# Optimization experiments

Measured on AMD Instinct MI355X. Metric: run time of the kernel, lower is better.

## Reference

```python
import jax, jax.numpy as jnp
import numpy as np

B, S, H = 8, 2048, 1024
CHUNK = 64
INTER = 2048
BASE_LR = 0.01
MAX_GRAD_NORM = 1.0
EPS = 1e-6


def rmsnorm(x, w):
    return x * jax.lax.rsqrt(jnp.mean(x * x, axis=-1, keepdims=True) + EPS) * w


def mem_fwd(params, x):
    # 2-layer MLP memory with residual: x + RMSNorm(W1 @ silu(W0 @ x))
    w0, w1, ln = params
    h = jax.nn.silu(x @ w0.T)
    y = h @ w1.T
    return x + rmsnorm(y, ln)


def forward(x, wq_w, wk_w, wv_w, q_norm_w, k_norm_w, alpha_w, theta_w, eta_w, mem_w0, mem_w1, mem_ln_w):
    Bx, Sx, Hx = x.shape
    NC = Sx // CHUNK  # seq_len divisible by chunk_size here (no padding needed)
    xc = x.reshape(Bx, NC, CHUNK, Hx)
    xf = xc.reshape(Bx, NC, CHUNK * Hx)

    # adaptive coefficients per chunk
    alpha = jax.nn.sigmoid(jnp.mean(xf @ alpha_w.T, axis=0))   # (NC, 1)
    theta = jax.nn.sigmoid(xf @ theta_w.T) * BASE_LR           # (B, NC, 1) per-sample loss weights
    eta = jax.nn.sigmoid(jnp.mean(xf @ eta_w.T, axis=0))       # (NC, 1)
    beta = 1.0 - alpha

    k = rmsnorm(jax.nn.silu(xc @ wk_w.T), k_norm_w)  # (B, NC, C, H)
    v = jax.nn.silu(xc @ wv_w.T)                     # (B, NC, C, H)

    mem0 = (mem_w0, mem_w1, mem_ln_w)
    surp0 = jax.tree_util.tree_map(jnp.zeros_like, mem0)

    def step(carry, inp):
        mem, surp = carry
        k_c, v_c, th_c, eta_c, beta_c = inp  # k_c,v_c: (B,C,H); th_c: (B,1); eta_c,beta_c: (1,)

        def loss_fn(p):
            pred = mem_fwd(p, k_c)
            return jnp.mean((v_c - pred) ** 2 * th_c[:, :, None])

        grads = jax.grad(loss_fn)(mem)
        total = jnp.sqrt(sum(jnp.sum(g * g) for g in grads))
        clip = jax.lax.stop_gradient(jnp.minimum(MAX_GRAD_NORM / (total + 1e-6), 1.0))
        new_surp = tuple(eta_c * s_ - g * clip for s_, g in zip(surp, grads))
        new_mem = tuple(beta_c * m + ns for m, ns in zip(mem, new_surp))
        return (new_mem, new_surp), None

    xs = (jnp.swapaxes(k, 0, 1), jnp.swapaxes(v, 0, 1), jnp.swapaxes(theta, 0, 1), eta, beta)
    (mem_f, _), _ = jax.lax.scan(step, (mem0, surp0), xs)

    # retrieve with final memory weights
    q = rmsnorm(jax.nn.silu(x @ wq_w.T), q_norm_w)
    return mem_fwd(mem_f, q)


def setup_inputs() -> dict:
    key = jax.random.key(0)
    ks = jax.random.split(key, 9)
    s = 0.02
    return {
        "x": jax.random.normal(ks[0], (B, S, H), jnp.float32),
        "wq_w": jax.random.normal(ks[1], (H, H), jnp.float32) * s,
        "wk_w": jax.random.normal(ks[2], (H, H), jnp.float32) * s,
        "wv_w": jax.random.normal(ks[3], (H, H), jnp.float32) * s,
        "q_norm_w": jnp.ones((H,), jnp.float32),
        "k_norm_w": jnp.ones((H,), jnp.float32),
        "alpha_w": jax.random.normal(ks[4], (1, CHUNK * H), jnp.float32) * s,
        "theta_w": jax.random.normal(ks[5], (1, CHUNK * H), jnp.float32) * s,
        "eta_w": jax.random.normal(ks[6], (1, CHUNK * H), jnp.float32) * s,
        "mem_w0": jax.random.normal(ks[7], (INTER, H), jnp.float32) * s,
        "mem_w1": jax.random.normal(ks[8], (H, INTER), jnp.float32) * s,
        "mem_ln_w": jnp.ones((H,), jnp.float32),
    }


def reference(x, wq_w, wk_w, wv_w, q_norm_w, k_norm_w, alpha_w, theta_w, eta_w, mem_w0, mem_w1, mem_ln_w):
    return forward(x, wq_w, wk_w, wv_w, q_norm_w, k_norm_w, alpha_w, theta_w, eta_w, mem_w0, mem_w1, mem_ln_w)
```

## Files before the change

### kernel.cpp

```cpp
#include <hip/hip_runtime.h>

#define HD 1024
#define ID 2048
#define NCHUNK 32
#define CHUNKSZ 64
#define NB 8
#define SEQ 2048
#define ROWS 512
#define MTOT 524288.0f
#define EPSF 1e-6f

typedef unsigned short u16;
typedef unsigned int u32;
typedef short bf16x8 __attribute__((ext_vector_type(8)));
typedef float f32x4 __attribute__((ext_vector_type(4)));

#define GATHER(r, c) ((((r) >> 6) * SEQ) + ((c) * CHUNKSZ) + ((r) & 63))

__device__ __forceinline__ float sigmoidf_(float x) { return 1.f / (1.f + expf(-x)); }
__device__ __forceinline__ float siluf_(float x)    { return x / (1.f + expf(-x)); }
__device__ __forceinline__ float silu_d_(float z)   { float sg = sigmoidf_(z); return sg * (1.f + z * (1.f - sg)); }

__device__ __forceinline__ u16 f2b(float f) {
  union { float f; u32 u; } v; v.f = f;
  return (u16)((v.u + 0x7fffu + ((v.u >> 16) & 1u)) >> 16);
}
__device__ __forceinline__ float b2f(u16 b) {
  union { u32 u; float f; } v; v.u = ((u32)b) << 16; return v.f;
}
__device__ __forceinline__ u32 pack2(float a, float b) { return (u32)f2b(a) | ((u32)f2b(b) << 16); }

__device__ __forceinline__ float block_reduce_sum(float v, float* s4) {
  #pragma unroll
  for (int off = 32; off > 0; off >>= 1) v += __shfl_down(v, off);
  int lane = threadIdx.x & 63, wid = threadIdx.x >> 6;
  if (lane == 0) s4[wid] = v;
  __syncthreads();
  float r = s4[0] + s4[1] + s4[2] + s4[3];
  __syncthreads();
  return r;
}

template<bool T>
__device__ __forceinline__ void stage64(u16* S, int srow, int c16, const uint4& r0, const uint4& r1) {
  if (!T) {
    *(uint4*)(S + srow * 72 + c16)     = r0;
    *(uint4*)(S + srow * 72 + c16 + 8) = r1;
  } else {
    const u16* e0 = (const u16*)&r0;
    const u16* e1 = (const u16*)&r1;
    #pragma unroll
    for (int e = 0; e < 8; ++e) S[(c16 + e) * 72 + srow] = e0[e];
    #pragma unroll
    for (int e = 0; e < 8; ++e) S[(c16 + 8 + e) * 72 + srow] = e1[e];
  }
}

template<bool AT, bool BT>
__device__ __forceinline__ void gemm64_db(
    f32x4 (&acc)[2][2], const u16* __restrict__ A, const u16* __restrict__ B,
    int K, int m0, int n0, int lda, int ldb, int chA, int chB,
    u16* As, u16* Bs)
{
  const int tid = threadIdx.x;
  const int lane = tid & 63, wave = tid >> 6;
  const int wr = wave >> 1, wc = wave & 1;
  const int l15 = lane & 15, q = lane >> 4;
  const int srow = tid >> 2, c16 = (tid & 3) * 16;

  const u16* Ap; size_t Astep;
  if (!AT) {
    int r = m0 + srow;
    if (chA >= 0) r = GATHER(r, chA);
    Ap = A + (size_t)r * lda + c16;
    Astep = 64;
  } else {
    Ap = A + (size_t)srow * lda + m0 + c16;
    Astep = (size_t)64 * lda;
  }
  const u16* Bp; size_t Bstep;
  if (!BT) {
    Bp = B + (size_t)(n0 + srow) * ldb + c16;
    Bstep = 64;
  } else {
    if (chB >= 0) { Bp = B + ((size_t)chB * CHUNKSZ + srow) * ldb + n0 + c16; Bstep = (size_t)SEQ * ldb; }
    else          { Bp = B + (size_t)srow * ldb + n0 + c16;                   Bstep = (size_t)64 * ldb; }
  }

  uint4 ra0 = *(const uint4*)Ap, ra1 = *(const uint4*)(Ap + 8);
  uint4 rb0 = *(const uint4*)Bp, rb1 = *(const uint4*)(Bp + 8);
  stage64<AT>(As, srow, c16, ra0, ra1);
  stage64<BT>(Bs, srow, c16, rb0, rb1);

  const int nt = K >> 6;
  int cur = 0;
  for (int t = 0; t < nt; ++t) {
    if (t + 1 < nt) {
      Ap += Astep; Bp += Bstep;
      ra0 = *(const uint4*)Ap; ra1 = *(const uint4*)(Ap + 8);
      rb0 = *(const uint4*)Bp; rb1 = *(const uint4*)(Bp + 8);
    }
    __syncthreads();
    const u16* Ac = As + cur * (64 * 72);
    const u16* Bc = Bs + cur * (64 * 72);
    #pragma unroll
    for (int ks = 0; ks < 2; ++ks) {
      bf16x8 af[2], bg[2];
      #pragma unroll
      for (int i = 0; i < 2; ++i) af[i] = *(const bf16x8*)&Ac[(wr * 32 + i * 16 + l15) * 72 + ks * 32 + q * 8];
      #pragma unroll
      for (int j = 0; j < 2; ++j) bg[j] = *(const bf16x8*)&Bc[(wc * 32 + j * 16 + l15) * 72 + ks * 32 + q * 8];
      #pragma unroll
      for (int i = 0; i < 2; ++i)
        #pragma unroll
        for (int j = 0; j < 2; ++j)
          acc[i][j] = __builtin_amdgcn_mfma_f32_16x16x32_bf16(af[i], bg[j], acc[i][j], 0, 0, 0);
    }
    if (t + 1 < nt) {
      stage64<AT>(As + (cur ^ 1) * (64 * 72), srow, c16, ra0, ra1);
      stage64<BT>(Bs + (cur ^ 1) * (64 * 72), srow, c16, rb0, rb1);
    }
    cur ^= 1;
  }
}

__global__ __launch_bounds__(256) void gemm64_fwd(
    float* __restrict__ C, u16* __restrict__ Cb,
    const u16* __restrict__ A, const u16* __restrict__ B, int N, int K, int chunk)
{
  __shared__ __align__(16) u16 As[2 * 64 * 72];
  __shared__ __align__(16) u16 Bs[2 * 64 * 72];
  const int m0 = blockIdx.y * 64, n0 = blockIdx.x * 64;
  f32x4 acc[2][2] = {};
  gemm64_db<false, false>(acc, A, B, K, m0, n0, K, K, chunk, -1, As, Bs);
  const int lane = threadIdx.x & 63, wave = threadIdx.x >> 6;
  const int wr = wave >> 1, wc = wave & 1;
  const int l15 = lane & 15, q = lane >> 4;
  #pragma unroll
  for (int i = 0; i < 2; ++i) {
    int r = m0 + wr * 32 + i * 16 + q * 4;
    #pragma unroll
    for (int j = 0; j < 2; ++j) {
      int col = n0 + wc * 32 + j * 16 + l15;
      #pragma unroll
      for (int t = 0; t < 4; ++t) {
        float v = acc[i][j][t];
        size_t o = (size_t)(r + t) * N + col;
        C[o] = v;
        Cb[o] = f2b(siluf_(v));
      }
    }
  }
}

__global__ __launch_bounds__(256) void gemm64_dh(
    u16* __restrict__ Cb, const u16* __restrict__ A, const u16* __restrict__ B,
    const float* __restrict__ Z, int N, int K)
{
  __shared__ __align__(16) u16 As[2 * 64 * 72];
  __shared__ __align__(16) u16 Bs[2 * 64 * 72];
  const int m0 = blockIdx.y * 64, n0 = blockIdx.x * 64;
  f32x4 acc[2][2] = {};
  gemm64_db<false, true>(acc, A, B, K, m0, n0, K, N, -1, -1, As, Bs);
  const int lane = threadIdx.x & 63, wave = threadIdx.x >> 6;
  const int wr = wave >> 1, wc = wave & 1;
  const int l15 = lane & 15, q = lane >> 4;
  #pragma unroll
  for (int i = 0; i < 2; ++i) {
    int r = m0 + wr * 32 + i * 16 + q * 4;
    #pragma unroll
    for (int j = 0; j < 2; ++j) {
      int col = n0 + wc * 32 + j * 16 + l15;
      #pragma unroll
      for (int t = 0; t < 4; ++t) {
        size_t o = (size_t)(r + t) * N + col;
        Cb[o] = f2b(acc[i][j][t] * silu_d_(Z[o]));
      }
    }
  }
}

__global__ __launch_bounds__(256) void gemm_grads(
    float* __restrict__ Gw1, const u16* __restrict__ dY, const u16* __restrict__ hfw,
    float* __restrict__ Gw0, const u16* __restrict__ dH, const u16* __restrict__ kall,
    int c, const float* __restrict__ g, const float* __restrict__ y,
    const float* __restrict__ srow, float* __restrict__ Gln, float* __restrict__ nsqc)
{
  __shared__ __align__(16) u16 As[2 * 64 * 72];
  __shared__ __align__(16) u16 Bs[2 * 64 * 72];
  __shared__ float s4[4];
  int bid = blockIdx.x;
  const int tid = threadIdx.x;
  if (bid >= 1024) {
    int j = (bid - 1024) * 32 + (tid & 31);
    int rg = tid >> 5;
    float acc = 0.f;
    #pragma unroll 4
    for (int i = 0; i < 64; ++i) {
      int r = rg * 64 + i;
      size_t o = (size_t)r * HD + j;
      acc += g[o] * y[o] * srow[r];
    }
    float* part = (float*)As;
    part[rg * 32 + (tid & 31)] = acc;
    __syncthreads();
    if (tid < 32) {
      float tot = 0.f;
      #pragma unroll
      for (int k = 0; k < 8; ++k) tot += part[k * 32 + tid];
      Gln[j] = tot;
      float sq = tot * tot;
      #pragma unroll
      for (int off = 16; off > 0; off >>= 1) sq += __shfl_down(sq, off);
      if (tid == 0) atomicAdd(nsqc, sq);
    }
    return;
  }
  float* C; const u16* A; const u16* B; int N, m0, n0, lda, ldb, chB;
  if (bid < 512) { A = dY; B = hfw;  C = Gw1; N = ID; lda = HD; ldb = ID; chB = -1; m0 = (bid >> 5) * 64; n0 = (bid & 31) * 64; }
  else { bid -= 512; A = dH; B = kall; C = Gw0; N = HD; lda = ID; ldb = HD; chB = c; m0 = (bid >> 4) * 64; n0 = (bid & 15) * 64; }
  f32x4 acc[2][2] = {};
  gemm64_db<true, true>(acc, A, B, ROWS, m0, n0, lda, ldb, -1, chB, As, Bs);
  const int lane = tid & 63, wave = tid >> 6;
  const int wr = wave >> 1, wc = wave & 1;
  const int l15 = lane & 15, q = lane >> 4;
  float ssq = 0.f;
  #pragma unroll
  for (int i = 0; i < 2; ++i) {
    int r = m0 + wr * 32 + i * 16 + q * 4;
    #pragma unroll
    for (int j = 0; j < 2; ++j) {
      int col = n0 + wc * 32 + j * 16 + l15;
      #pragma unroll
      for (int t = 0; t < 4; ++t) {
        float v = acc[i][j][t];
        C[(size_t)(r + t) * N + col] = v;
        ssq += v * v;
      }
    }
  }
  float tot = block_reduce_sum(ssq, s4);
  if (tid == 0) atomicAdd(nsqc, tot);
}

__global__ __launch_bounds__(128) void gemm_y32(
    float* __restrict__ C, const u16* __restrict__ A, const u16* __restrict__ B,
    int N, int K)
{
  __shared__ __align__(16) u16 As[2 * 32 * 72];
  __shared__ __align__(16) u16 Bs[2 * 64 * 72];
  const int tid = threadIdx.x;
  const int lane = tid & 63, wc = tid >> 6;
  const int l15 = lane & 15, q = lane >> 4;
  const int m0 = blockIdx.y * 32, n0 = blockIdx.x * 64;

  const int arow = tid >> 2, ac16 = (tid & 3) * 16;
  const int brow = tid >> 1, bc32 = (tid & 1) * 32;
  const u16* Ap = A + (size_t)(m0 + arow) * K + ac16;
  const u16* Bp = B + (size_t)(n0 + brow) * K + bc32;

  uint4 ra0 = *(const uint4*)Ap, ra1 = *(const uint4*)(Ap + 8);
  uint4 rb0 = *(const uint4*)Bp, rb1 = *(const uint4*)(Bp + 8);
  uint4 rb2 = *(const uint4*)(Bp + 16), rb3 = *(const uint4*)(Bp + 24);
  {
    u16* Aw = As + arow * 72 + ac16;
    u16* Bw = Bs + brow * 72 + bc32;
    *(uint4*)Aw = ra0; *(uint4*)(Aw + 8) = ra1;
    *(uint4*)Bw = rb0; *(uint4*)(Bw + 8) = rb1;
    *(uint4*)(Bw + 16) = rb2; *(uint4*)(Bw + 24) = rb3;
  }

  f32x4 acc[2][2] = {};
  const int nt = K >> 6;
  int cur = 0;
  for (int t = 0; t < nt; ++t) {
    if (t + 1 < nt) {
      Ap += 64; Bp += 64;
      ra0 = *(const uint4*)Ap; ra1 = *(const uint4*)(Ap + 8);
      rb0 = *(const uint4*)Bp; rb1 = *(const uint4*)(Bp + 8);
      rb2 = *(const uint4*)(Bp + 16); rb3 = *(const uint4*)(Bp + 24);
    }
    __syncthreads();
    const u16* Ac = As + cur * (32 * 72);
    const u16* Bc = Bs + cur * (64 * 72);
    #pragma unroll
    for (int ks = 0; ks < 2; ++ks) {
      bf16x8 af[2], bg[2];
      #pragma unroll
      for (int i = 0; i < 2; ++i) af[i] = *(const bf16x8*)&Ac[(i * 16 + l15) * 72 + ks * 32 + q * 8];
      #pragma unroll
      for (int j = 0; j < 2; ++j) bg[j] = *(const bf16x8*)&Bc[(wc * 32 + j * 16 + l15) * 72 + ks * 32 + q * 8];
      #pragma unroll
      for (int i = 0; i < 2; ++i)
        #pragma unroll
        for (int j = 0; j < 2; ++j)
          acc[i][j] = __builtin_amdgcn_mfma_f32_16x16x32_bf16(af[i], bg[j], acc[i][j], 0, 0, 0);
    }
    if (t + 1 < nt) {
      u16* Aw = As + (cur ^ 1) * (32 * 72) + arow * 72 + ac16;
      u16* Bw = Bs + (cur ^ 1) * (64 * 72) + brow * 72 + bc32;
      *(uint4*)Aw = ra0; *(uint4*)(Aw + 8) = ra1;
      *(uint4*)Bw = rb0; *(uint4*)(Bw + 8) = rb1;
      *(uint4*)(Bw + 16) = rb2; *(uint4*)(Bw + 24) = rb3;
    }
    cur ^= 1;
  }
  #pragma unroll
  for (int i = 0; i < 2; ++i) {
    int r = m0 + i * 16 + q * 4;
    #pragma unroll
    for (int j = 0; j < 2; ++j) {
      int col = n0 + wc * 32 + j * 16 + l15;
      #pragma unroll
      for (int t = 0; t < 4; ++t)
        C[(size_t)(r + t) * N + col] = acc[i][j][t];
    }
  }
}

template<int EPI, bool AF32>
__global__ __launch_bounds__(256) void gemm128_t(
    float* __restrict__ C, u16* __restrict__ Cb, u16* __restrict__ Cb1,
    const u16* __restrict__ A, const float* __restrict__ Af,
    const u16* __restrict__ B0, const u16* __restrict__ B1,
    int M, int N, int K)
{
  __shared__ __align__(16) u16 As[128 * 40];
  __shared__ __align__(16) u16 Bs[128 * 40];
  const int tid = threadIdx.x;
  const int lane = tid & 63, wave = tid >> 6;
  const int wr = wave >> 1, wc = wave & 1;
  const int l15 = lane & 15, q = lane >> 4;
  const int m0 = blockIdx.y * 128, n0 = blockIdx.x * 128;
  const u16* B = (EPI == 2 && blockIdx.z) ? B1 : B0;

  f32x4 acc[4][4] = {};
  for (int k0 = 0; k0 < K; k0 += 32) {
    #pragma unroll
    for (int it = 0; it < 2; ++it) {
      int cid = tid + it * 256;
      int row = cid >> 2, c8 = (cid & 3) * 8;
      if (AF32) {
        const float* ap = Af + (size_t)(m0 + row) * K + k0 + c8;
        float4 f0 = *(const float4*)ap;
        float4 f1 = *(const float4*)(ap + 4);
        uint4 o; o.x = pack2(f0.x, f0.y); o.y = pack2(f0.z, f0.w);
        o.z = pack2(f1.x, f1.y); o.w = pack2(f1.z, f1.w);
        *(uint4*)&As[row * 40 + c8] = o;
      } else {
        *(uint4*)&As[row * 40 + c8] = *(const uint4*)&A[(size_t)(m0 + row) * K + k0 + c8];
      }
      *(uint4*)&Bs[row * 40 + c8] = *(const uint4*)&B[(size_t)(n0 + row) * K + k0 + c8];
    }
    __syncthreads();
    bf16x8 af[4], bg[4];
    #pragma unroll
    for (int i = 0; i < 4; ++i) af[i] = *(const bf16x8*)&As[(wr * 64 + i * 16 + l15) * 40 + q * 8];
    #pragma unroll
    for (int j = 0; j < 4; ++j) bg[j] = *(const bf16x8*)&Bs[(wc * 64 + j * 16 + l15) * 40 + q * 8];
    #pragma unroll
    for (int i = 0; i < 4; ++i)
      #pragma unroll
      for (int j = 0; j < 4; ++j)
        acc[i][j] = __builtin_amdgcn_mfma_f32_16x16x32_bf16(af[i], bg[j], acc[i][j], 0, 0, 0);
    __syncthreads();
  }
  #pragma unroll
  for (int i = 0; i < 4; ++i) {
    int r = m0 + wr * 64 + i * 16 + q * 4;
    #pragma unroll
    for (int j = 0; j < 4; ++j) {
      int col = n0 + wc * 64 + j * 16 + l15;
      #pragma unroll
      for (int t = 0; t < 4; ++t) {
        float v = acc[i][j][t];
        size_t o = (size_t)(r + t) * N + col;
        if (EPI == 0) C[o] = v;
        if (EPI == 1) Cb[o] = f2b(siluf_(v));
        if (EPI == 2) { if (blockIdx.z == 0) Cb[o] = f2b(v); else Cb1[o] = f2b(siluf_(v)); }
      }
    }
  }
}

__global__ __launch_bounds__(256) void conv_f2b(u16* __restrict__ dst, const float* __restrict__ src, int n) {
  int i = (blockIdx.x * 256 + threadIdx.x) * 4;
  if (i < n) {
    float4 v = *(const float4*)&src[i];
    uint2 o; o.x = pack2(v.x, v.y); o.y = pack2(v.z, v.w);
    *(uint2*)&dst[i] = o;
  }
}

__global__ __launch_bounds__(256) void dots_kernel(
    const float* __restrict__ x, const float* __restrict__ aw,
    const float* __restrict__ tw, const float* __restrict__ ew,
    float* __restrict__ dA, float* __restrict__ dT, float* __restrict__ dE)
{
  int b = blockIdx.x >> 5, c = blockIdx.x & 31;
  const float* base = x + ((size_t)b * SEQ + (size_t)c * CHUNKSZ) * HD;
  float a = 0.f, t = 0.f, e = 0.f;
  for (int it = 0; it < 64; ++it) {
    int j = (it * 256 + threadIdx.x) * 4;
    float4 xv = *(const float4*)&base[j];
    float4 av = *(const float4*)&aw[j];
    float4 tv = *(const float4*)&tw[j];
    float4 ev = *(const float4*)&ew[j];
    a += xv.x * av.x + xv.y * av.y + xv.z * av.z + xv.w * av.w;
    t += xv.x * tv.x + xv.y * tv.y + xv.z * tv.z + xv.w * tv.w;
    e += xv.x * ev.x + xv.y * ev.y + xv.z * ev.z + xv.w * ev.w;
  }
  __shared__ float s4[4];
  a = block_reduce_sum(a, s4);
  t = block_reduce_sum(t, s4);
  e = block_reduce_sum(e, s4);
  if (threadIdx.x == 0) { dA[blockIdx.x] = a; dT[blockIdx.x] = t; dE[blockIdx.x] = e; }
}

__global__ __launch_bounds__(256) void coeff_kernel(
    const float* __restrict__ dA, const float* __restrict__ dT, const float* __restrict__ dE,
    float* __restrict__ betaA, float* __restrict__ etaA, float* __restrict__ thetaA)
{
  int t = threadIdx.x;
  if (t < 256) thetaA[t] = sigmoidf_(dT[t]) * 0.01f;
  if (t < 32) {
    float sa = 0.f, se = 0.f;
    for (int b = 0; b < NB; ++b) { sa += dA[b * 32 + t]; se += dE[b * 32 + t]; }
    betaA[t] = 1.f - sigmoidf_(sa / 8.f);
    etaA[t]  = sigmoidf_(se / 8.f);
  }
}

template<bool SRCB>
__global__ __launch_bounds__(256) void post_norm(
    u16* __restrict__ dstb, const float* __restrict__ srcf,
    const u16* __restrict__ srcb, const float* __restrict__ nw)
{
  size_t off = (size_t)blockIdx.x * HD;
  float sv[4]; float ss = 0.f;
  #pragma unroll
  for (int i = 0; i < 4; ++i) {
    int j = i * 256 + threadIdx.x;
    float z = SRCB ? b2f(srcb[off + j]) : srcf[off + j];
    float s = siluf_(z);
    sv[i] = s; ss += s * s;
  }
  __shared__ float s4[4];
  ss = block_reduce_sum(ss, s4);
  float rs = rsqrtf(ss / (float)HD + EPSF);
  #pragma unroll
  for (int i = 0; i < 4; ++i) {
    int j = i * 256 + threadIdx.x;
    dstb[off + j] = f2b(sv[i] * rs * nw[j]);
  }
}

__global__ __launch_bounds__(256) void loss_grad(
    const float* __restrict__ y, const u16* __restrict__ kall, const u16* __restrict__ vall,
    const float* __restrict__ ln, const float* __restrict__ thetaA, int c,
    float* __restrict__ g, u16* __restrict__ dYbf, float* __restrict__ srow)
{
  int r = blockIdx.x;
  size_t off = (size_t)r * HD;
  size_t goff = (size_t)GATHER(r, c) * HD;
  float th = thetaA[(r >> 6) * 32 + c];
  float yv[4], lnv[4];
  float ss = 0.f;
  #pragma unroll
  for (int i = 0; i < 4; ++i) {
    int j = i * 256 + threadIdx.x;
    yv[i] = y[off + j];
    lnv[i] = ln[j];
    ss += yv[i] * yv[i];
  }
  __shared__ float s4[4];
  ss = block_reduce_sum(ss, s4);
  float s = rsqrtf(ss / (float)HD + EPSF);
  float coef = 2.f * th / MTOT;
  float gv[4]; float t = 0.f;
  #pragma unroll
  for (int i = 0; i < 4; ++i) {
    int j = i * 256 + threadIdx.x;
    float pred = b2f(kall[goff + j]) + yv[i] * s * lnv[i];
    float gg = coef * (pred - b2f(vall[goff + j]));
    gv[i] = gg;
    g[off + j] = gg;
    t += gg * lnv[i] * yv[i];
  }
  t = block_reduce_sum(t, s4);
  float c3 = s * s * s * t * (1.f / (float)HD);
  #pragma unroll
  for (int i = 0; i < 4; ++i) {
    int j = i * 256 + threadIdx.x;
    dYbf[off + j] = f2b(s * gv[i] * lnv[i] - c3 * yv[i]);
  }
  if (threadIdx.x == 0) srow[r] = s;
}

__global__ __launch_bounds__(256) void update_all(
    float* __restrict__ mw0, float* __restrict__ sw0, const float* __restrict__ g0, u16* __restrict__ w0b,
    float* __restrict__ mw1, float* __restrict__ sw1, const float* __restrict__ g1, u16* __restrict__ w1b,
    float* __restrict__ mln, float* __restrict__ sln, const float* __restrict__ gl,
    const float* __restrict__ etaA, const float* __restrict__ betaA, int c,
    const float* __restrict__ nsqc)
{
  float clip = fminf(1.0f / (sqrtf(*nsqc) + 1e-6f), 1.0f);
  float eta = etaA[c], beta = betaA[c];
  int bid = blockIdx.x;
  if (bid < 2048) {
    float* mw; float* sw; const float* g; u16* wb; size_t i0;
    if (bid < 1024) { mw = mw1; sw = sw1; g = g1; wb = w1b; i0 = (size_t)bid * 2048; }
    else            { mw = mw0; sw = sw0; g = g0; wb = w0b; i0 = (size_t)(bid - 1024) * 2048; }
    i0 += (size_t)threadIdx.x * 8;
    u16 bb[8];
    #pragma unroll
    for (int h = 0; h < 2; ++h) {
      size_t i = i0 + h * 4;
      float4 s = *(float4*)&sw[i];
      float4 gg = *(const float4*)&g[i];
      float4 m = *(float4*)&mw[i];
      s.x = eta * s.x - clip * gg.x; m.x = beta * m.x + s.x;
      s.y = eta * s.y - clip * gg.y; m.y = beta * m.y + s.y;
      s.z = eta * s.z - clip * gg.z; m.z = beta * m.z + s.z;
      s.w = eta * s.w - clip * gg.w; m.w = beta * m.w + s.w;
      *(float4*)&sw[i] = s;
      *(float4*)&mw[i] = m;
      bb[h * 4 + 0] = f2b(m.x); bb[h * 4 + 1] = f2b(m.y);
      bb[h * 4 + 2] = f2b(m.z); bb[h * 4 + 3] = f2b(m.w);
    }
    *(uint4*)&wb[i0] = *(uint4*)bb;
  } else {
    int i = threadIdx.x * 4;
    #pragma unroll
    for (int k = 0; k < 4; ++k) {
      float ns = eta * sln[i + k] - clip * gl[i + k];
      sln[i + k] = ns;
      mln[i + k] = beta * mln[i + k] + ns;
    }
  }
}

__global__ __launch_bounds__(256) void final_out_kernel(
    float* __restrict__ out, const float* __restrict__ zq, const float* __restrict__ y2,
    const float* __restrict__ qn, const float* __restrict__ ln)
{
  size_t off = (size_t)blockIdx.x * HD;
  float sv[4], yv[4];
  float ss1 = 0.f, ss2 = 0.f;
  #pragma unroll
  for (int i = 0; i < 4; ++i) {
    int j = i * 256 + threadIdx.x;
    float s = siluf_(zq[off + j]);
    sv[i] = s; ss1 += s * s;
    yv[i] = y2[off + j];
    ss2 += yv[i] * yv[i];
  }
  __shared__ float s4[4];
  ss1 = block_reduce_sum(ss1, s4);
  ss2 = block_reduce_sum(ss2, s4);
  float rs1 = rsqrtf(ss1 / (float)HD + EPSF);
  float rs2 = rsqrtf(ss2 / (float)HD + EPSF);
  #pragma unroll
  for (int i = 0; i < 4; ++i) {
    int j = i * 256 + threadIdx.x;
    out[off + j] = sv[i] * rs1 * qn[j] + yv[i] * rs2 * ln[j];
  }
}

extern "C" void kernel_launch(void* const* d_in, const int* in_sizes, int n_in,
                              void* d_out, int out_size, void* d_ws, size_t ws_size,
                              hipStream_t stream) {
  const float* x   = (const float*)d_in[0];
  const float* wq  = (const float*)d_in[1];
  const float* wk  = (const float*)d_in[2];
  const float* wv  = (const float*)d_in[3];
  const float* qn  = (const float*)d_in[4];
  const float* kn  = (const float*)d_in[5];
  const float* aw  = (const float*)d_in[6];
  const float* tw  = (const float*)d_in[7];
  const float* ew  = (const float*)d_in[8];
  const float* w0i = (const float*)d_in[9];
  const float* w1i = (const float*)d_in[10];
  const float* lni = (const float*)d_in[11];
  float* out = (float*)d_out;

  float* p = (float*)d_ws;
  auto alloc = [&](size_t n) { n = (n + 63) & ~(size_t)63; float* r = p; p += n; return r; };
  float* memW0  = alloc((size_t)ID * HD);
  float* memW1  = alloc((size_t)HD * ID);
  float* memLn  = alloc(HD);
  float* surpW0 = alloc((size_t)ID * HD);
  float* surpW1 = alloc((size_t)HD * ID);
  float* surpLn = alloc(HD);
  float* Gw0    = alloc((size_t)ID * HD);
  float* Gw1    = alloc((size_t)HD * ID);
  float* Gln    = alloc(HD);
  float* zfw    = alloc((size_t)ROWS * ID);
  float* ybuf   = alloc((size_t)ROWS * HD);
  float* gbuf   = alloc((size_t)ROWS * HD);
  float* srow   = alloc(ROWS);
  float* dotA   = alloc(256);
  float* dotT   = alloc(256);
  float* dotE   = alloc(256);
  float* betaA  = alloc(64);
  float* etaA   = alloc(64);
  float* thetaA = alloc(256);
  float* nsq    = alloc(64);

  u16* bp = (u16*)p;
  auto balloc = [&](size_t n) { n = (n + 63) & ~(size_t)63; u16* r = bp; bp += n; return r; };
  u16* wq_bf  = balloc((size_t)HD * HD);
  u16* wk_bf  = balloc((size_t)HD * HD);
  u16* wv_bf  = balloc((size_t)HD * HD);
  u16* W0_bf  = balloc((size_t)ID * HD);
  u16* W1_bf  = balloc((size_t)HD * ID);
  u16* k_all  = balloc((size_t)NB * SEQ * HD);
  u16* v_all  = balloc((size_t)NB * SEQ * HD);
  u16* hfw_bf = balloc((size_t)ROWS * ID);
  u16* dY_bf  = balloc((size_t)ROWS * HD);
  u16* dH_bf  = balloc((size_t)ROWS * ID);
  size_t needed = (size_t)((char*)bp - (char*)d_ws);
  if (needed > ws_size) return;

  u16* zk_all = (u16*)surpW0;

  conv_f2b<<<(HD * HD) / 1024, 256, 0, stream>>>(wq_bf, wq, HD * HD);
  conv_f2b<<<(HD * HD) / 1024, 256, 0, stream>>>(wk_bf, wk, HD * HD);
  conv_f2b<<<(HD * HD) / 1024, 256, 0, stream>>>(wv_bf, wv, HD * HD);
  conv_f2b<<<(ID * HD) / 1024, 256, 0, stream>>>(W0_bf, w0i, ID * HD);
  conv_f2b<<<(HD * ID) / 1024, 256, 0, stream>>>(W1_bf, w1i, HD * ID);
  dots_kernel<<<256, 256, 0, stream>>>(x, aw, tw, ew, dotA, dotT, dotE);
  coeff_kernel<<<1, 256, 0, stream>>>(dotA, dotT, dotE, betaA, etaA, thetaA);
  gemm128_t<2, true><<<dim3(HD / 128, (NB * SEQ) / 128, 2), 256, 0, stream>>>(
      nullptr, zk_all, v_all, nullptr, x, wk_bf, wv_bf, NB * SEQ, HD, HD);
  post_norm<true><<<NB * SEQ, 256, 0, stream>>>(k_all, nullptr, zk_all, kn);
  hipMemcpyAsync(memW0, w0i, (size_t)ID * HD * 4, hipMemcpyDeviceToDevice, stream);
  hipMemcpyAsync(memW1, w1i, (size_t)HD * ID * 4, hipMemcpyDeviceToDevice, stream);
  hipMemcpyAsync(memLn, lni, (size_t)HD * 4, hipMemcpyDeviceToDevice, stream);
  hipMemsetAsync(surpW0, 0, ((size_t)ID * HD * 2 + HD + 64) * 4, stream);
  hipMemsetAsync(nsq, 0, 64 * 4, stream);

  for (int c = 0; c < NCHUNK; ++c) {
    gemm64_fwd<<<dim3(ID / 64, ROWS / 64), 256, 0, stream>>>(
        zfw, hfw_bf, k_all, W0_bf, ID, HD, c);
    gemm_y32<<<dim3(HD / 64, ROWS / 32), 128, 0, stream>>>(ybuf, hfw_bf, W1_bf, HD, ID);
    loss_grad<<<ROWS, 256, 0, stream>>>(ybuf, k_all, v_all, memLn, thetaA, c, gbuf, dY_bf, srow);
    gemm64_dh<<<dim3(ID / 64, ROWS / 64), 256, 0, stream>>>(
        dH_bf, dY_bf, W1_bf, zfw, ID, HD);
    gemm_grads<<<1056, 256, 0, stream>>>(
        Gw1, dY_bf, hfw_bf, Gw0, dH_bf, k_all, c, gbuf, ybuf, srow, Gln, nsq + c);
    update_all<<<2049, 256, 0, stream>>>(
        memW0, surpW0, Gw0, W0_bf, memW1, surpW1, Gw1, W1_bf,
        memLn, surpLn, Gln, etaA, betaA, c, nsq + c);
  }

  const int RB = 4096;
  float* zq    = surpW0;
  u16*   qb_bf = (u16*)zfw;
  u16*   h_bf  = k_all;
  float* y2    = Gw0;
  for (int blk = 0; blk < (NB * SEQ) / RB; ++blk) {
    const float* xb = x + (size_t)blk * RB * HD;
    gemm128_t<0, true><<<dim3(HD / 128, RB / 128), 256, 0, stream>>>(
        zq, nullptr, nullptr, nullptr, xb, wq_bf, nullptr, RB, HD, HD);
    post_norm<false><<<RB, 256, 0, stream>>>(qb_bf, zq, nullptr, qn);
    gemm128_t<1, false><<<dim3(ID / 128, RB / 128), 256, 0, stream>>>(
        nullptr, h_bf, nullptr, qb_bf, nullptr, W0_bf, nullptr, RB, ID, HD);
    gemm128_t<0, false><<<dim3(HD / 128, RB / 128), 256, 0, stream>>>(
        y2, nullptr, nullptr, h_bf, nullptr, W1_bf, nullptr, RB, HD, ID);
    final_out_kernel<<<RB, 256, 0, stream>>>(out + (size_t)blk * RB * HD, zq, y2, qn, memLn);
  }
}
```

Measured before the change: 3.698 ms.

## Split-K the per-chunk GEMMs and fuse the Q/K/V projections

The per-chunk forward, dh and y GEMMs now use larger blocks that split the K dimension across two or four thread groups and reduce the partial sums through shared memory. This is meant to put more waves to work on the small 512-row scan GEMMs, at the cost of extra LDS traffic and barriers. Separately, x is converted to bf16 once and the Q, K and V projections run in one XCD-aware GEMM launch; the q norm is computed early and stored in the output buffer. The retrieval GEMMs are then processed in larger row blocks using specialised kernels.

```diff
diff --git a/kernel.cpp b/kernel.cpp
--- a/kernel.cpp
+++ b/kernel.cpp
@@ -124,57 +124,152 @@
   }
 }
 
-__global__ __launch_bounds__(256) void gemm64_fwd(
+template<bool BT>
+__device__ __forceinline__ void gemm64x8(
+    f32x4 (&acc)[2][2], const u16* __restrict__ A, const u16* __restrict__ B,
+    int K, int m0, int n0, int lda, int ldb, int chA, u16* As, u16* Bs)
+{
+  const int tid = threadIdx.x;
+  const int half = tid >> 8;
+  const int t2 = tid & 255;
+  const int lane = tid & 63;
+  const int w2 = t2 >> 6;
+  const int wr = w2 >> 1, wc = w2 & 1;
+  const int l15 = lane & 15, q = lane >> 4;
+  const int srow = t2 >> 2, c16 = (t2 & 3) * 16;
+  const int kbase = half * (K >> 1);
+
+  int arow = m0 + srow;
+  if (chA >= 0) arow = GATHER(arow, chA);
+  const u16* Ap = A + (size_t)arow * lda + kbase + c16;
+  const u16* Bp; size_t Bstep;
+  if (!BT) { Bp = B + (size_t)(n0 + srow) * ldb + kbase + c16; Bstep = 64; }
+  else     { Bp = B + (size_t)(kbase + srow) * ldb + n0 + c16; Bstep = (size_t)64 * ldb; }
+
+  u16* Ah = As + half * (2 * 64 * 72);
+  u16* Bh = Bs + half * (2 * 64 * 72);
+
+  uint4 ra0 = *(const uint4*)Ap, ra1 = *(const uint4*)(Ap + 8);
+  uint4 rb0 = *(const uint4*)Bp, rb1 = *(const uint4*)(Bp + 8);
+  stage64<false>(Ah, srow, c16, ra0, ra1);
+  stage64<BT>(Bh, srow, c16, rb0, rb1);
+
+  const int nt = K >> 7;
+  int cur = 0;
+  for (int t = 0; t < nt; ++t) {
+    if (t + 1 < nt) {
+      Ap += 64; Bp += Bstep;
+      ra0 = *(const uint4*)Ap; ra1 = *(const uint4*)(Ap + 8);
+      rb0 = *(const uint4*)Bp; rb1 = *(const uint4*)(Bp + 8);
+    }
+    __syncthreads();
+    const u16* Ac = Ah + cur * (64 * 72);
+    const u16* Bc = Bh + cur * (64 * 72);
+    #pragma unroll
+    for (int ks = 0; ks < 2; ++ks) {
+      bf16x8 af[2], bg[2];
+      #pragma unroll
+      for (int i = 0; i < 2; ++i) af[i] = *(const bf16x8*)&Ac[(wr * 32 + i * 16 + l15) * 72 + ks * 32 + q * 8];
+      #pragma unroll
+      for (int j = 0; j < 2; ++j) bg[j] = *(const bf16x8*)&Bc[(wc * 32 + j * 16 + l15) * 72 + ks * 32 + q * 8];
+      #pragma unroll
+      for (int i = 0; i < 2; ++i)
+        #pragma unroll
+        for (int j = 0; j < 2; ++j)
+          acc[i][j] = __builtin_amdgcn_mfma_f32_16x16x32_bf16(af[i], bg[j], acc[i][j], 0, 0, 0);
+    }
+    if (t + 1 < nt) {
+      stage64<false>(Ah + (cur ^ 1) * (64 * 72), srow, c16, ra0, ra1);
+      stage64<BT>(Bh + (cur ^ 1) * (64 * 72), srow, c16, rb0, rb1);
+    }
+    cur ^= 1;
+  }
+}
+
+__global__ __launch_bounds__(512) void gemm64_fwd(
     float* __restrict__ C, u16* __restrict__ Cb,
     const u16* __restrict__ A, const u16* __restrict__ B, int N, int K, int chunk)
 {
-  __shared__ __align__(16) u16 As[2 * 64 * 72];
-  __shared__ __align__(16) u16 Bs[2 * 64 * 72];
+  __shared__ __align__(16) u16 As[2 * 2 * 64 * 72];
+  __shared__ __align__(16) u16 Bs[2 * 2 * 64 * 72];
   const int m0 = blockIdx.y * 64, n0 = blockIdx.x * 64;
   f32x4 acc[2][2] = {};
-  gemm64_db<false, false>(acc, A, B, K, m0, n0, K, K, chunk, -1, As, Bs);
-  const int lane = threadIdx.x & 63, wave = threadIdx.x >> 6;
-  const int wr = wave >> 1, wc = wave & 1;
-  const int l15 = lane & 15, q = lane >> 4;
-  #pragma unroll
-  for (int i = 0; i < 2; ++i) {
-    int r = m0 + wr * 32 + i * 16 + q * 4;
-    #pragma unroll
-    for (int j = 0; j < 2; ++j) {
-      int col = n0 + wc * 32 + j * 16 + l15;
-      #pragma unroll
-      for (int t = 0; t < 4; ++t) {
-        float v = acc[i][j][t];
-        size_t o = (size_t)(r + t) * N + col;
-        C[o] = v;
-        Cb[o] = f2b(siluf_(v));
+  gemm64x8<false>(acc, A, B, K, m0, n0, K, K, chunk, As, Bs);
+  const int tid = threadIdx.x;
+  const int half = tid >> 8, t2 = tid & 255;
+  const int lane = tid & 63, w2 = t2 >> 6;
+  const int wr = w2 >> 1, wc = w2 & 1;
+  const int l15 = lane & 15, q = lane >> 4;
+  float* Cm = (float*)As;
+  __syncthreads();
+  if (half) {
+    #pragma unroll
+    for (int i = 0; i < 2; ++i)
+      #pragma unroll
+      for (int j = 0; j < 2; ++j)
+        #pragma unroll
+        for (int t = 0; t < 4; ++t)
+          Cm[(wr * 32 + i * 16 + q * 4 + t) * 66 + wc * 32 + j * 16 + l15] = acc[i][j][t];
+  }
+  __syncthreads();
+  if (!half) {
+    #pragma unroll
+    for (int i = 0; i < 2; ++i) {
+      int r = m0 + wr * 32 + i * 16 + q * 4;
+      #pragma unroll
+      for (int j = 0; j < 2; ++j) {
+        int col = n0 + wc * 32 + j * 16 + l15;
+        #pragma unroll
+        for (int t = 0; t < 4; ++t) {
+          float v = acc[i][j][t] + Cm[(wr * 32 + i * 16 + q * 4 + t) * 66 + wc * 32 + j * 16 + l15];
+          size_t o = (size_t)(r + t) * N + col;
+          C[o] = v;
+          Cb[o] = f2b(siluf_(v));
+        }
       }
     }
   }
 }
 
-__global__ __launch_bounds__(256) void gemm64_dh(
+__global__ __launch_bounds__(512) void gemm64_dh(
     u16* __restrict__ Cb, const u16* __restrict__ A, const u16* __restrict__ B,
     const float* __restrict__ Z, int N, int K)
 {
-  __shared__ __align__(16) u16 As[2 * 64 * 72];
-  __shared__ __align__(16) u16 Bs[2 * 64 * 72];
+  __shared__ __align__(16) u16 As[2 * 2 * 64 * 72];
+  __shared__ __align__(16) u16 Bs[2 * 2 * 64 * 72];
   const int m0 = blockIdx.y * 64, n0 = blockIdx.x * 64;
   f32x4 acc[2][2] = {};
-  gemm64_db<false, true>(acc, A, B, K, m0, n0, K, N, -1, -1, As, Bs);
-  const int lane = threadIdx.x & 63, wave = threadIdx.x >> 6;
-  const int wr = wave >> 1, wc = wave & 1;
-  const int l15 = lane & 15, q = lane >> 4;
-  #pragma unroll
-  for (int i = 0; i < 2; ++i) {
-    int r = m0 + wr * 32 + i * 16 + q * 4;
-    #pragma unroll
-    for (int j = 0; j < 2; ++j) {
-      int col = n0 + wc * 32 + j * 16 + l15;
-      #pragma unroll
-      for (int t = 0; t < 4; ++t) {
-        size_t o = (size_t)(r + t) * N + col;
-        Cb[o] = f2b(acc[i][j][t] * silu_d_(Z[o]));
+  gemm64x8<true>(acc, A, B, K, m0, n0, K, N, -1, As, Bs);
+  const int tid = threadIdx.x;
+  const int half = tid >> 8, t2 = tid & 255;
+  const int lane = tid & 63, w2 = t2 >> 6;
+  const int wr = w2 >> 1, wc = w2 & 1;
+  const int l15 = lane & 15, q = lane >> 4;
+  float* Cm = (float*)As;
+  __syncthreads();
+  if (half) {
+    #pragma unroll
+    for (int i = 0; i < 2; ++i)
+      #pragma unroll
+      for (int j = 0; j < 2; ++j)
+        #pragma unroll
+        for (int t = 0; t < 4; ++t)
+          Cm[(wr * 32 + i * 16 + q * 4 + t) * 66 + wc * 32 + j * 16 + l15] = acc[i][j][t];
+  }
+  __syncthreads();
+  if (!half) {
+    #pragma unroll
+    for (int i = 0; i < 2; ++i) {
+      int r = m0 + wr * 32 + i * 16 + q * 4;
+      #pragma unroll
+      for (int j = 0; j < 2; ++j) {
+        int col = n0 + wc * 32 + j * 16 + l15;
+        #pragma unroll
+        for (int t = 0; t < 4; ++t) {
+          float v = acc[i][j][t] + Cm[(wr * 32 + i * 16 + q * 4 + t) * 66 + wc * 32 + j * 16 + l15];
+          size_t o = (size_t)(r + t) * N + col;
+          Cb[o] = f2b(v * silu_d_(Z[o]));
+        }
       }
     }
   }
@@ -243,35 +338,41 @@
   if (tid == 0) atomicAdd(nsqc, tot);
 }
 
-__global__ __launch_bounds__(128) void gemm_y32(
+__global__ __launch_bounds__(512) void gemm_y32(
     float* __restrict__ C, const u16* __restrict__ A, const u16* __restrict__ B,
     int N, int K)
 {
-  __shared__ __align__(16) u16 As[2 * 32 * 72];
-  __shared__ __align__(16) u16 Bs[2 * 64 * 72];
-  const int tid = threadIdx.x;
-  const int lane = tid & 63, wc = tid >> 6;
+  __shared__ __align__(16) u16 As[4 * 2 * 32 * 72];
+  __shared__ __align__(16) u16 Bs[4 * 2 * 64 * 72];
+  const int tid = threadIdx.x;
+  const int qt = tid >> 7;
+  const int t2 = tid & 127;
+  const int lane = tid & 63;
+  const int wc = t2 >> 6;
   const int l15 = lane & 15, q = lane >> 4;
   const int m0 = blockIdx.y * 32, n0 = blockIdx.x * 64;
-
-  const int arow = tid >> 2, ac16 = (tid & 3) * 16;
-  const int brow = tid >> 1, bc32 = (tid & 1) * 32;
-  const u16* Ap = A + (size_t)(m0 + arow) * K + ac16;
-  const u16* Bp = B + (size_t)(n0 + brow) * K + bc32;
+  const int kbase = qt * (K >> 2);
+
+  const int arow = t2 >> 2, ac16 = (t2 & 3) * 16;
+  const int brow = t2 >> 1, bc32 = (t2 & 1) * 32;
+  const u16* Ap = A + (size_t)(m0 + arow) * K + kbase + ac16;
+  const u16* Bp = B + (size_t)(n0 + brow) * K + kbase + bc32;
+  u16* Aq = As + qt * (2 * 32 * 72);
+  u16* Bq = Bs + qt * (2 * 64 * 72);
 
   uint4 ra0 = *(const uint4*)Ap, ra1 = *(const uint4*)(Ap + 8);
   uint4 rb0 = *(const uint4*)Bp, rb1 = *(const uint4*)(Bp + 8);
   uint4 rb2 = *(const uint4*)(Bp + 16), rb3 = *(const uint4*)(Bp + 24);
   {
-    u16* Aw = As + arow * 72 + ac16;
-    u16* Bw = Bs + brow * 72 + bc32;
+    u16* Aw = Aq + arow * 72 + ac16;
+    u16* Bw = Bq + brow * 72 + bc32;
     *(uint4*)Aw = ra0; *(uint4*)(Aw + 8) = ra1;
     *(uint4*)Bw = rb0; *(uint4*)(Bw + 8) = rb1;
     *(uint4*)(Bw + 16) = rb2; *(uint4*)(Bw + 24) = rb3;
   }
 
   f32x4 acc[2][2] = {};
-  const int nt = K >> 6;
+  const int nt = K >> 8;
   int cur = 0;
   for (int t = 0; t < nt; ++t) {
     if (t + 1 < nt) {
@@ -281,8 +382,8 @@
       rb2 = *(const uint4*)(Bp + 16); rb3 = *(const uint4*)(Bp + 24);
     }
     __syncthreads();
-    const u16* Ac = As + cur * (32 * 72);
-    const u16* Bc = Bs + cur * (64 * 72);
+    const u16* Ac = Aq + cur * (32 * 72);
+    const u16* Bc = Bq + cur * (64 * 72);
     #pragma unroll
     for (int ks = 0; ks < 2; ++ks) {
       bf16x8 af[2], bg[2];
@@ -297,60 +398,62 @@
           acc[i][j] = __builtin_amdgcn_mfma_f32_16x16x32_bf16(af[i], bg[j], acc[i][j], 0, 0, 0);
     }
     if (t + 1 < nt) {
-      u16* Aw = As + (cur ^ 1) * (32 * 72) + arow * 72 + ac16;
-      u16* Bw = Bs + (cur ^ 1) * (64 * 72) + brow * 72 + bc32;
+      u16* Aw = Aq + (cur ^ 1) * (32 * 72) + arow * 72 + ac16;
+      u16* Bw = Bq + (cur ^ 1) * (64 * 72) + brow * 72 + bc32;
       *(uint4*)Aw = ra0; *(uint4*)(Aw + 8) = ra1;
       *(uint4*)Bw = rb0; *(uint4*)(Bw + 8) = rb1;
       *(uint4*)(Bw + 16) = rb2; *(uint4*)(Bw + 24) = rb3;
     }
     cur ^= 1;
   }
-  #pragma unroll
-  for (int i = 0; i < 2; ++i) {
-    int r = m0 + i * 16 + q * 4;
-    #pragma unroll
-    for (int j = 0; j < 2; ++j) {
-      int col = n0 + wc * 32 + j * 16 + l15;
-      #pragma unroll
-      for (int t = 0; t < 4; ++t)
-        C[(size_t)(r + t) * N + col] = acc[i][j][t];
-    }
-  }
-}
-
-template<int EPI, bool AF32>
-__global__ __launch_bounds__(256) void gemm128_t(
-    float* __restrict__ C, u16* __restrict__ Cb, u16* __restrict__ Cb1,
-    const u16* __restrict__ A, const float* __restrict__ Af,
-    const u16* __restrict__ B0, const u16* __restrict__ B1,
-    int M, int N, int K)
-{
-  __shared__ __align__(16) u16 As[128 * 40];
-  __shared__ __align__(16) u16 Bs[128 * 40];
+  float* Cm = (float*)As;
+  __syncthreads();
+  if (qt) {
+    #pragma unroll
+    for (int i = 0; i < 2; ++i)
+      #pragma unroll
+      for (int j = 0; j < 2; ++j)
+        #pragma unroll
+        for (int t = 0; t < 4; ++t)
+          Cm[((qt - 1) * 32 + i * 16 + q * 4 + t) * 66 + wc * 32 + j * 16 + l15] = acc[i][j][t];
+  }
+  __syncthreads();
+  if (!qt) {
+    #pragma unroll
+    for (int i = 0; i < 2; ++i) {
+      int r = m0 + i * 16 + q * 4;
+      #pragma unroll
+      for (int j = 0; j < 2; ++j) {
+        int col = n0 + wc * 32 + j * 16 + l15;
+        #pragma unroll
+        for (int t = 0; t < 4; ++t) {
+          float v = acc[i][j][t];
+          #pragma unroll
+          for (int p = 0; p < 3; ++p)
+            v += Cm[(p * 32 + i * 16 + q * 4 + t) * 66 + wc * 32 + j * 16 + l15];
+          C[(size_t)(r + t) * N + col] = v;
+        }
+      }
+    }
+  }
+}
+
+__device__ __forceinline__ void gemm128_core(
+    f32x4 (&acc)[4][4], const u16* __restrict__ A, int lda,
+    const u16* __restrict__ B, int ldb, int K, int m0, int n0,
+    u16* As, u16* Bs)
+{
   const int tid = threadIdx.x;
   const int lane = tid & 63, wave = tid >> 6;
   const int wr = wave >> 1, wc = wave & 1;
   const int l15 = lane & 15, q = lane >> 4;
-  const int m0 = blockIdx.y * 128, n0 = blockIdx.x * 128;
-  const u16* B = (EPI == 2 && blockIdx.z) ? B1 : B0;
-
-  f32x4 acc[4][4] = {};
   for (int k0 = 0; k0 < K; k0 += 32) {
     #pragma unroll
     for (int it = 0; it < 2; ++it) {
       int cid = tid + it * 256;
       int row = cid >> 2, c8 = (cid & 3) * 8;
-      if (AF32) {
-        const float* ap = Af + (size_t)(m0 + row) * K + k0 + c8;
-        float4 f0 = *(const float4*)ap;
-        float4 f1 = *(const float4*)(ap + 4);
-        uint4 o; o.x = pack2(f0.x, f0.y); o.y = pack2(f0.z, f0.w);
-        o.z = pack2(f1.x, f1.y); o.w = pack2(f1.z, f1.w);
-        *(uint4*)&As[row * 40 + c8] = o;
-      } else {
-        *(uint4*)&As[row * 40 + c8] = *(const uint4*)&A[(size_t)(m0 + row) * K + k0 + c8];
-      }
-      *(uint4*)&Bs[row * 40 + c8] = *(const uint4*)&B[(size_t)(n0 + row) * K + k0 + c8];
+      *(uint4*)&As[row * 40 + c8] = *(const uint4*)&A[(size_t)(m0 + row) * lda + k0 + c8];
+      *(uint4*)&Bs[row * 40 + c8] = *(const uint4*)&B[(size_t)(n0 + row) * ldb + k0 + c8];
     }
     __syncthreads();
     bf16x8 af[4], bg[4];
@@ -365,6 +468,28 @@
         acc[i][j] = __builtin_amdgcn_mfma_f32_16x16x32_bf16(af[i], bg[j], acc[i][j], 0, 0, 0);
     __syncthreads();
   }
+}
+
+__global__ __launch_bounds__(256) void gemm_qkv(
+    float* __restrict__ zqC, u16* __restrict__ kC, u16* __restrict__ vC,
+    const u16* __restrict__ xb, const u16* __restrict__ wk,
+    const u16* __restrict__ wv, const u16* __restrict__ wq)
+{
+  __shared__ __align__(16) u16 As[128 * 40];
+  __shared__ __align__(16) u16 Bs[128 * 40];
+  int f = blockIdx.x;
+  int xcd = f & 7, jj = f >> 3;
+  int panel = xcd + 8 * (jj / 24);
+  int w = jj % 24;
+  int z = w >> 3, xt = w & 7;
+  int m0 = panel * 128, n0 = xt * 128;
+  const u16* B = (z == 0) ? wk : ((z == 1) ? wv : wq);
+  f32x4 acc[4][4] = {};
+  gemm128_core(acc, xb, HD, B, HD, HD, m0, n0, As, Bs);
+  const int tid = threadIdx.x;
+  const int lane = tid & 63, wave = tid >> 6;
+  const int wr = wave >> 1, wc = wave & 1;
+  const int l15 = lane & 15, q = lane >> 4;
   #pragma unroll
   for (int i = 0; i < 4; ++i) {
     int r = m0 + wr * 64 + i * 16 + q * 4;
@@ -374,11 +499,69 @@
       #pragma unroll
       for (int t = 0; t < 4; ++t) {
         float v = acc[i][j][t];
-        size_t o = (size_t)(r + t) * N + col;
-        if (EPI == 0) C[o] = v;
-        if (EPI == 1) Cb[o] = f2b(siluf_(v));
-        if (EPI == 2) { if (blockIdx.z == 0) Cb[o] = f2b(v); else Cb1[o] = f2b(siluf_(v)); }
+        size_t o = (size_t)(r + t) * HD + col;
+        if (z == 0) kC[o] = f2b(v);
+        else if (z == 1) vC[o] = f2b(siluf_(v));
+        else zqC[o] = v;
       }
+    }
+  }
+}
+
+__global__ __launch_bounds__(256) void gemm_h(
+    u16* __restrict__ hC, const u16* __restrict__ A, const u16* __restrict__ B)
+{
+  __shared__ __align__(16) u16 As[128 * 40];
+  __shared__ __align__(16) u16 Bs[128 * 40];
+  int f = blockIdx.x;
+  int xcd = f & 7, jj = f >> 3;
+  int panel = xcd + 8 * (jj >> 4);
+  int xt = jj & 15;
+  int m0 = panel * 128, n0 = xt * 128;
+  f32x4 acc[4][4] = {};
+  gemm128_core(acc, A, HD, B, HD, HD, m0, n0, As, Bs);
+  const int tid = threadIdx.x;
+  const int lane = tid & 63, wave = tid >> 6;
+  const int wr = wave >> 1, wc = wave & 1;
+  const int l15 = lane & 15, q = lane >> 4;
+  #pragma unroll
+  for (int i = 0; i < 4; ++i) {
+    int r = m0 + wr * 64 + i * 16 + q * 4;
+    #pragma unroll
+    for (int j = 0; j < 4; ++j) {
+      int col = n0 + wc * 64 + j * 16 + l15;
+      #pragma unroll
+      for (int t = 0; t < 4; ++t)
+        hC[(size_t)(r + t) * ID + col] = f2b(siluf_(acc[i][j][t]));
+    }
+  }
+}
+
+__global__ __launch_bounds__(256) void gemm_y2(
+    float* __restrict__ C, const u16* __restrict__ A, const u16* __restrict__ B)
+{
+  __shared__ __align__(16) u16 As[128 * 40];
+  __shared__ __align__(16) u16 Bs[128 * 40];
+  int f = blockIdx.x;
+  int xcd = f & 7, jj = f >> 3;
+  int panel = xcd + 8 * (jj >> 3);
+  int xt = jj & 7;
+  int m0 = panel * 128, n0 = xt * 128;
+  f32x4 acc[4][4] = {};
+  gemm128_core(acc, A, ID, B, ID, ID, m0, n0, As, Bs);
+  const int tid = threadIdx.x;
+  const int lane = tid & 63, wave = tid >> 6;
+  const int wr = wave >> 1, wc = wave & 1;
+  const int l15 = lane & 15, q = lane >> 4;
+  #pragma unroll
+  for (int i = 0; i < 4; ++i) {
+    int r = m0 + wr * 64 + i * 16 + q * 4;
+    #pragma unroll
+    for (int j = 0; j < 4; ++j) {
+      int col = n0 + wc * 64 + j * 16 + l15;
+      #pragma unroll
+      for (int t = 0; t < 4; ++t)
+        C[(size_t)(r + t) * HD + col] = acc[i][j][t];
     }
   }
 }
@@ -431,18 +614,14 @@
   }
 }
 
-template<bool SRCB>
-__global__ __launch_bounds__(256) void post_norm(
-    u16* __restrict__ dstb, const float* __restrict__ srcf,
-    const u16* __restrict__ srcb, const float* __restrict__ nw)
+__global__ __launch_bounds__(256) void post_norm_kb(u16* buf, const float* __restrict__ nw)
 {
   size_t off = (size_t)blockIdx.x * HD;
   float sv[4]; float ss = 0.f;
   #pragma unroll
   for (int i = 0; i < 4; ++i) {
     int j = i * 256 + threadIdx.x;
-    float z = SRCB ? b2f(srcb[off + j]) : srcf[off + j];
-    float s = siluf_(z);
+    float s = siluf_(b2f(buf[off + j]));
     sv[i] = s; ss += s * s;
   }
   __shared__ float s4[4];
@@ -451,7 +630,27 @@
   #pragma unroll
   for (int i = 0; i < 4; ++i) {
     int j = i * 256 + threadIdx.x;
-    dstb[off + j] = f2b(sv[i] * rs * nw[j]);
+    buf[off + j] = f2b(sv[i] * rs * nw[j]);
+  }
+}
+
+__global__ __launch_bounds__(256) void post_norm_qf(float* buf, const float* __restrict__ nw)
+{
+  size_t off = (size_t)blockIdx.x * HD;
+  float sv[4]; float ss = 0.f;
+  #pragma unroll
+  for (int i = 0; i < 4; ++i) {
+    int j = i * 256 + threadIdx.x;
+    float s = siluf_(buf[off + j]);
+    sv[i] = s; ss += s * s;
+  }
+  __shared__ float s4[4];
+  ss = block_reduce_sum(ss, s4);
+  float rs = rsqrtf(ss / (float)HD + EPSF);
+  #pragma unroll
+  for (int i = 0; i < 4; ++i) {
+    int j = i * 256 + threadIdx.x;
+    buf[off + j] = sv[i] * rs * nw[j];
   }
 }
 
@@ -541,29 +740,25 @@
 }
 
 __global__ __launch_bounds__(256) void final_out_kernel(
-    float* __restrict__ out, const float* __restrict__ zq, const float* __restrict__ y2,
-    const float* __restrict__ qn, const float* __restrict__ ln)
+    float* outp, const float* __restrict__ y2, const float* __restrict__ ln)
 {
   size_t off = (size_t)blockIdx.x * HD;
-  float sv[4], yv[4];
-  float ss1 = 0.f, ss2 = 0.f;
+  float qv[4], yv[4];
+  float ss2 = 0.f;
   #pragma unroll
   for (int i = 0; i < 4; ++i) {
     int j = i * 256 + threadIdx.x;
-    float s = siluf_(zq[off + j]);
-    sv[i] = s; ss1 += s * s;
+    qv[i] = outp[off + j];
     yv[i] = y2[off + j];
     ss2 += yv[i] * yv[i];
   }
   __shared__ float s4[4];
-  ss1 = block_reduce_sum(ss1, s4);
   ss2 = block_reduce_sum(ss2, s4);
-  float rs1 = rsqrtf(ss1 / (float)HD + EPSF);
   float rs2 = rsqrtf(ss2 / (float)HD + EPSF);
   #pragma unroll
   for (int i = 0; i < 4; ++i) {
     int j = i * 256 + threadIdx.x;
-    out[off + j] = sv[i] * rs1 * qn[j] + yv[i] * rs2 * ln[j];
+    outp[off + j] = qv[i] + yv[i] * rs2 * ln[j];
   }
 }
 
@@ -588,12 +783,12 @@
   auto alloc = [&](size_t n) { n = (n + 63) & ~(size_t)63; float* r = p; p += n; return r; };
   float* memW0  = alloc((size_t)ID * HD);
   float* memW1  = alloc((size_t)HD * ID);
-  float* memLn  = alloc(HD);
   float* surpW0 = alloc((size_t)ID * HD);
   float* surpW1 = alloc((size_t)HD * ID);
-  float* surpLn = alloc(HD);
   float* Gw0    = alloc((size_t)ID * HD);
   float* Gw1    = alloc((size_t)HD * ID);
+  float* memLn  = alloc(HD);
+  float* surpLn = alloc(HD);
   float* Gln    = alloc(HD);
   float* zfw    = alloc((size_t)ROWS * ID);
   float* ybuf   = alloc((size_t)ROWS * HD);
@@ -622,30 +817,32 @@
   size_t needed = (size_t)((char*)bp - (char*)d_ws);
   if (needed > ws_size) return;
 
-  u16* zk_all = (u16*)surpW0;
+  u16* x_bf = (u16*)memW0;
 
   conv_f2b<<<(HD * HD) / 1024, 256, 0, stream>>>(wq_bf, wq, HD * HD);
   conv_f2b<<<(HD * HD) / 1024, 256, 0, stream>>>(wk_bf, wk, HD * HD);
   conv_f2b<<<(HD * HD) / 1024, 256, 0, stream>>>(wv_bf, wv, HD * HD);
   conv_f2b<<<(ID * HD) / 1024, 256, 0, stream>>>(W0_bf, w0i, ID * HD);
   conv_f2b<<<(HD * ID) / 1024, 256, 0, stream>>>(W1_bf, w1i, HD * ID);
+  conv_f2b<<<(NB * SEQ * HD) / 1024, 256, 0, stream>>>(x_bf, x, NB * SEQ * HD);
   dots_kernel<<<256, 256, 0, stream>>>(x, aw, tw, ew, dotA, dotT, dotE);
   coeff_kernel<<<1, 256, 0, stream>>>(dotA, dotT, dotE, betaA, etaA, thetaA);
-  gemm128_t<2, true><<<dim3(HD / 128, (NB * SEQ) / 128, 2), 256, 0, stream>>>(
-      nullptr, zk_all, v_all, nullptr, x, wk_bf, wv_bf, NB * SEQ, HD, HD);
-  post_norm<true><<<NB * SEQ, 256, 0, stream>>>(k_all, nullptr, zk_all, kn);
+  gemm_qkv<<<3072, 256, 0, stream>>>(out, k_all, v_all, x_bf, wk_bf, wv_bf, wq_bf);
+  post_norm_kb<<<NB * SEQ, 256, 0, stream>>>(k_all, kn);
+  post_norm_qf<<<NB * SEQ, 256, 0, stream>>>(out, qn);
   hipMemcpyAsync(memW0, w0i, (size_t)ID * HD * 4, hipMemcpyDeviceToDevice, stream);
   hipMemcpyAsync(memW1, w1i, (size_t)HD * ID * 4, hipMemcpyDeviceToDevice, stream);
   hipMemcpyAsync(memLn, lni, (size_t)HD * 4, hipMemcpyDeviceToDevice, stream);
-  hipMemsetAsync(surpW0, 0, ((size_t)ID * HD * 2 + HD + 64) * 4, stream);
+  hipMemsetAsync(surpW0, 0, (size_t)ID * HD * 2 * 4, stream);
+  hipMemsetAsync(surpLn, 0, HD * 4, stream);
   hipMemsetAsync(nsq, 0, 64 * 4, stream);
 
   for (int c = 0; c < NCHUNK; ++c) {
-    gemm64_fwd<<<dim3(ID / 64, ROWS / 64), 256, 0, stream>>>(
+    gemm64_fwd<<<dim3(ID / 64, ROWS / 64), 512, 0, stream>>>(
         zfw, hfw_bf, k_all, W0_bf, ID, HD, c);
-    gemm_y32<<<dim3(HD / 64, ROWS / 32), 128, 0, stream>>>(ybuf, hfw_bf, W1_bf, HD, ID);
+    gemm_y32<<<dim3(HD / 64, ROWS / 32), 512, 0, stream>>>(ybuf, hfw_bf, W1_bf, HD, ID);
     loss_grad<<<ROWS, 256, 0, stream>>>(ybuf, k_all, v_all, memLn, thetaA, c, gbuf, dY_bf, srow);
-    gemm64_dh<<<dim3(ID / 64, ROWS / 64), 256, 0, stream>>>(
+    gemm64_dh<<<dim3(ID / 64, ROWS / 64), 512, 0, stream>>>(
         dH_bf, dY_bf, W1_bf, zfw, ID, HD);
     gemm_grads<<<1056, 256, 0, stream>>>(
         Gw1, dY_bf, hfw_bf, Gw0, dH_bf, k_all, c, gbuf, ybuf, srow, Gln, nsq + c);
@@ -654,20 +851,13 @@
         memLn, surpLn, Gln, etaA, betaA, c, nsq + c);
   }
 
-  const int RB = 4096;
-  float* zq    = surpW0;
-  u16*   qb_bf = (u16*)zfw;
-  u16*   h_bf  = k_all;
-  float* y2    = Gw0;
-  for (int blk = 0; blk < (NB * SEQ) / RB; ++blk) {
-    const float* xb = x + (size_t)blk * RB * HD;
-    gemm128_t<0, true><<<dim3(HD / 128, RB / 128), 256, 0, stream>>>(
-        zq, nullptr, nullptr, nullptr, xb, wq_bf, nullptr, RB, HD, HD);
-    post_norm<false><<<RB, 256, 0, stream>>>(qb_bf, zq, nullptr, qn);
-    gemm128_t<1, false><<<dim3(ID / 128, RB / 128), 256, 0, stream>>>(
-        nullptr, h_bf, nullptr, qb_bf, nullptr, W0_bf, nullptr, RB, ID, HD);
-    gemm128_t<0, false><<<dim3(HD / 128, RB / 128), 256, 0, stream>>>(
-        y2, nullptr, nullptr, h_bf, nullptr, W1_bf, nullptr, RB, HD, ID);
-    final_out_kernel<<<RB, 256, 0, stream>>>(out + (size_t)blk * RB * HD, zq, y2, qn, memLn);
-  }
-}
+  u16*   qb_bf = k_all;
+  u16*   h_bf  = v_all;
+  float* y2    = surpW0;
+  conv_f2b<<<(NB * SEQ * HD) / 1024, 256, 0, stream>>>(qb_bf, out, NB * SEQ * HD);
+  for (int blk = 0; blk < 2; ++blk) {
+    gemm_h<<<1024, 256, 0, stream>>>(h_bf, qb_bf + (size_t)blk * 8192 * HD, W0_bf);
+    gemm_y2<<<512, 256, 0, stream>>>(y2, h_bf, W1_bf);
+    final_out_kernel<<<8192, 256, 0, stream>>>(out + (size_t)blk * 8192 * HD, y2, memLn);
+  }
+}
```

Measured after the change: 3.106 ms. 16.0% less time.
